# Kernel tuning notes

Measured on AMD Instinct MI355X. Metric: run time of the kernel, lower is better.

The kernel has to match this reference:

```python
import jax, jax.numpy as jnp
import numpy as np
from jax import lax

START = 0  # label_dict['<START>']
END = 8    # label_dict['<END>']
NEG = -10000.0


def setup_inputs() -> dict:
    key = jax.random.key(0)
    k1, k2, k3 = jax.random.split(key, 3)
    B, S, C = 8192, 512, 9
    emission = jax.random.normal(k1, (B, S, C), dtype=jnp.float32)
    # transition_matrix ~ normal, then START row / END column masked to -10000
    T = jax.random.normal(k2, (C, C), dtype=jnp.float32)
    T = T.at[START, :].set(NEG).at[:, END].set(NEG)
    labels = jax.random.randint(k3, (B, S), 0, 8, dtype=jnp.int32)
    mask = jnp.ones((B, S), dtype=jnp.int32)
    return {"emission": emission, "transition": T, "labels": labels, "mask": mask}


def _log_partition(emission, T, mask_f):
    # emission: [B,S,C], T: [C,C], mask_f: [B,S] float
    B, S, C = emission.shape
    init = jnp.full((B, C), NEG, dtype=emission.dtype).at[:, 0].set(0.0)

    def step(log_alpha, inp):
        em_t, m_t = inp  # [B,C], [B,1]
        # add[b,i,j] = log_alpha[b,i] + em_t[b,j] + T[i,j]
        add = log_alpha[:, :, None] + em_t[:, None, :] + T[None, :, :]
        new = jax.nn.logsumexp(add, axis=1)  # [B,C]
        log_alpha = new * m_t + log_alpha * (1.0 - m_t)
        return log_alpha, None

    em_sw = jnp.swapaxes(emission, 0, 1)          # [S,B,C]
    m_sw = jnp.swapaxes(mask_f, 0, 1)[:, :, None]  # [S,B,1]
    final, _ = lax.scan(step, init, (em_sw, m_sw))
    final = final + T[:, END][None, :]
    return jax.nn.logsumexp(final, axis=1)  # [B]


def _sentence_score(emission, T, labels, mask_f):
    B, S, C = emission.shape
    # prepend <START>=0 label
    labels_ext = jnp.concatenate(
        [jnp.full((B, 1), START, dtype=labels.dtype), labels], axis=1)  # [B,S+1]
    # emission score at the gold label of each position
    emit = jnp.take_along_axis(emission, labels[:, :, None].astype(jnp.int32), axis=2)[..., 0]  # [B,S]
    trans = T[labels_ext[:, :-1], labels_ext[:, 1:]]  # [B,S]
    scores = jnp.sum((emit + trans) * mask_f, axis=1)  # [B]
    lengths = jnp.sum(mask_f, axis=1).astype(jnp.int32)  # [B]
    last_label = labels_ext[jnp.arange(B), lengths]       # label at position len in ext seq
    scores = scores + T[last_label, END]
    return scores


def reference(emission, transition, labels, mask):
    mask_f = mask.astype(emission.dtype)
    log_Z = _log_partition(emission, transition, mask_f)
    gold = _sentence_score(emission, transition, labels, mask_f)
    loss = jnp.mean(log_Z - gold)
    return loss
```

## Files before the change

### kernel.cpp

```cpp
#include <hip/hip_runtime.h>


#define CC 9
#define SS 512
#define GPW 7
#define BLOCKT 64
#define NEGV (-10000.0f)

__device__ __forceinline__ float bperm_f(int idx, float v) {
    return __int_as_float(__builtin_amdgcn_ds_bpermute(idx, __float_as_int(v)));
}

struct Chunk {
    float em[8];
    int4 lab0, lab1, msk0, msk1;
};

struct CrfState {
    float q, offset, goldem, goldtr;
    int prev, len;
};

__device__ __forceinline__ void load_chunk(Chunk& c, const float* emp,
                                           const int* labp, const int* mskp, int t0) {
#pragma unroll
    for (int k = 0; k < 8; ++k) c.em[k] = emp[(t0 + k) * CC];
    c.lab0 = *(const int4*)(labp + t0);
    c.lab1 = *(const int4*)(labp + t0 + 4);
    c.msk0 = *(const int4*)(mskp + t0);
    c.msk1 = *(const int4*)(mskp + t0 + 4);
}

template <bool RENORM>
__device__ __forceinline__ void crf_step(CrfState& st, float em_t, int lab_t, int msk_t,
                                         const float* Tl, const float* ecol,
                                         int idxbase, int j) {
    float g[CC];
#pragma unroll
    for (int i = 0; i < CC; ++i) g[i] = bperm_f(idxbase + 4 * i, st.q);

    float e = __expf(em_t);
    float tv = Tl[st.prev * CC + lab_t];
    bool m = (msk_t != 0);
    st.goldtr += m ? tv : 0.0f;
    st.goldem += (m && (lab_t == j)) ? em_t : 0.0f;
    st.len += m ? 1 : 0;
    st.prev = lab_t;

    float s0 = g[0] * ecol[0];
    float s1 = g[1] * ecol[1];
    float s2 = g[2] * ecol[2];
    s0 = fmaf(g[3], ecol[3], s0);
    s1 = fmaf(g[4], ecol[4], s1);
    s2 = fmaf(g[5], ecol[5], s2);
    s0 = fmaf(g[6], ecol[6], s0);
    s1 = fmaf(g[7], ecol[7], s1);
    s2 = fmaf(g[8], ecol[8], s2);
    float s = s0 + s1 + s2;

    float nq = m ? s * e : st.q;
    if (RENORM) {
        float mx = fmaxf(fmaxf(fmaxf(g[0], g[1]), fmaxf(g[2], g[3])),
                         fmaxf(fmaxf(g[4], g[5]),
                               fmaxf(g[6], fmaxf(g[7], g[8]))));
        nq = nq / mx;
        st.offset += __logf(mx);
    }
    st.q = nq;
}

__device__ __forceinline__ void consume8(CrfState& st, const Chunk& c, const float* Tl,
                                         const float* ecol, int idxbase, int j) {
    crf_step<true >(st, c.em[0], c.lab0.x, c.msk0.x, Tl, ecol, idxbase, j);
    crf_step<false>(st, c.em[1], c.lab0.y, c.msk0.y, Tl, ecol, idxbase, j);
    crf_step<false>(st, c.em[2], c.lab0.z, c.msk0.z, Tl, ecol, idxbase, j);
    crf_step<false>(st, c.em[3], c.lab0.w, c.msk0.w, Tl, ecol, idxbase, j);
    crf_step<true >(st, c.em[4], c.lab1.x, c.msk1.x, Tl, ecol, idxbase, j);
    crf_step<false>(st, c.em[5], c.lab1.y, c.msk1.y, Tl, ecol, idxbase, j);
    crf_step<false>(st, c.em[6], c.lab1.z, c.msk1.z, Tl, ecol, idxbase, j);
    crf_step<false>(st, c.em[7], c.lab1.w, c.msk1.w, Tl, ecol, idxbase, j);
}

__global__ void zero_out_kernel(float* out) { out[0] = 0.0f; }

__global__ __launch_bounds__(BLOCKT) void crf_main(
    const float* __restrict__ emission, const float* __restrict__ transition,
    const int* __restrict__ labels, const int* __restrict__ mask,
    float* __restrict__ out, int B, float invB) {
    __shared__ float Tl[CC * CC];
    int tid = threadIdx.x;
    for (int i = tid; i < CC * CC; i += BLOCKT) Tl[i] = transition[i];
    __syncthreads();

    int lane = tid & 63;
    int grp = lane / CC;
    int j = lane - grp * CC;
    long batch = (long)blockIdx.x * GPW + grp;
    bool valid = (grp < GPW) && (batch < (long)B);
    int idxbase = (grp * CC) * 4;

    float ecol[CC];
#pragma unroll
    for (int i = 0; i < CC; ++i) ecol[i] = __expf(Tl[i * CC + j]);
    float mT8 = Tl[0 * CC + 8];
#pragma unroll
    for (int i = 1; i < CC; ++i) mT8 = fmaxf(mT8, Tl[i * CC + 8]);
    float wend = __expf(Tl[j * CC + 8] - mT8);

    float vj, vref;
    {
        float mxj = Tl[j], mx0 = Tl[0];
#pragma unroll
        for (int i = 1; i < CC; ++i) {
            mxj = fmaxf(mxj, NEGV + Tl[i * CC + j]);
            mx0 = fmaxf(mx0, NEGV + Tl[i * CC + 0]);
        }
        float sj = __expf(Tl[j] - mxj), s0 = __expf(Tl[0] - mx0);
#pragma unroll
        for (int i = 1; i < CC; ++i) {
            sj += __expf(NEGV + Tl[i * CC + j] - mxj);
            s0 += __expf(NEGV + Tl[i * CC + 0] - mx0);
        }
        vj = mxj + __logf(sj);
        vref = mx0 + __logf(s0);
    }

    size_t bidx = valid ? (size_t)batch : 0;
    const float* emp = emission + bidx * (SS * CC) + j;
    const int* labp = labels + bidx * SS;
    const int* mskp = mask + bidx * SS;

    CrfState st;
    st.q = 0.f; st.offset = 0.f; st.goldem = 0.f; st.goldtr = 0.f;
    st.prev = 0; st.len = 0;

    Chunk A, Bc;
    load_chunk(A, emp, labp, mskp, 0);
    load_chunk(Bc, emp, labp, mskp, 8);

    {
        float em0 = A.em[0];
        int lab0 = A.lab0.x;
        bool m0 = (A.msk0.x != 0);
        st.offset = m0 ? vref : 0.f;
        st.q = m0 ? __expf(vj + em0 - vref) : ((j == 0) ? 1.f : 0.f);
        st.goldtr = m0 ? Tl[lab0] : 0.f;
        st.goldem = (m0 && lab0 == j) ? em0 : 0.f;
        st.len = m0 ? 1 : 0;
        st.prev = lab0;
    }
    crf_step<false>(st, A.em[1], A.lab0.y, A.msk0.y, Tl, ecol, idxbase, j);
    crf_step<false>(st, A.em[2], A.lab0.z, A.msk0.z, Tl, ecol, idxbase, j);
    crf_step<false>(st, A.em[3], A.lab0.w, A.msk0.w, Tl, ecol, idxbase, j);
    crf_step<true >(st, A.em[4], A.lab1.x, A.msk1.x, Tl, ecol, idxbase, j);
    crf_step<false>(st, A.em[5], A.lab1.y, A.msk1.y, Tl, ecol, idxbase, j);
    crf_step<false>(st, A.em[6], A.lab1.z, A.msk1.z, Tl, ecol, idxbase, j);
    crf_step<false>(st, A.em[7], A.lab1.w, A.msk1.w, Tl, ecol, idxbase, j);

    load_chunk(A, emp, labp, mskp, 16);

    for (int c = 1; c <= 61; c += 2) {
        consume8(st, Bc, Tl, ecol, idxbase, j);
        load_chunk(Bc, emp, labp, mskp, (c + 2) * 8);
        consume8(st, A, Tl, ecol, idxbase, j);
        if (c + 3 <= 63) load_chunk(A, emp, labp, mskp, (c + 3) * 8);
    }
    consume8(st, Bc, Tl, ecol, idxbase, j);

    int lastlab = 0;
    if (st.len > 0) lastlab = labp[st.len - 1];
    float gend = Tl[lastlab * CC + 8];
    float fin = st.q * wend;
    float gpart = st.goldem + ((j == 0) ? (st.goldtr + gend) : 0.f);
    float sw = 0.f, sg = 0.f;
#pragma unroll
    for (int i = 0; i < CC; ++i) {
        sw += bperm_f(idxbase + 4 * i, fin);
        sg += bperm_f(idxbase + 4 * i, gpart);
    }
    if (valid && j == 0) {
        float logZ = st.offset + mT8 + __logf(sw);
        atomicAdd(out, (logZ - sg) * invB);
    }
}

extern "C" void kernel_launch(void* const* d_in, const int* in_sizes, int n_in,
                              void* d_out, int out_size, void* d_ws, size_t ws_size,
                              hipStream_t stream) {
    const float* emission = (const float*)d_in[0];
    const float* transition = (const float*)d_in[1];
    const int* labels = (const int*)d_in[2];
    const int* mask = (const int*)d_in[3];
    float* out = (float*)d_out;

    int B = in_sizes[2] / SS;
    float invB = 1.0f / (float)B;

    zero_out_kernel<<<1, 1, 0, stream>>>(out);
    int nblocks = (B + GPW - 1) / GPW;
    crf_main<<<nblocks, BLOCKT, 0, stream>>>(emission, transition, labels, mask,
                                             out, B, invB);
}
```

Measured before the change: 279.9 us.

## Fold CRF states onto 8 lanes, use DPP rotates, reduce per block

```diff
diff --git a/kernel.cpp b/kernel.cpp
--- a/kernel.cpp
+++ b/kernel.cpp
@@ -3,185 +3,216 @@
 
 #define CC 9
 #define SS 512
-#define GPW 7
-#define BLOCKT 64
 #define NEGV (-10000.0f)
-
-__device__ __forceinline__ float bperm_f(int idx, float v) {
-    return __int_as_float(__builtin_amdgcn_ds_bpermute(idx, __float_as_int(v)));
+#define BLOCKT 256
+#define BPW 8
+#define BPB 32
+
+template <int M>
+__device__ __forceinline__ float rotf(float v) {
+    return __int_as_float(__builtin_amdgcn_update_dpp(
+        0, __float_as_int(v), 0x120 + 2 * M, 0xF, 0xF, false));
+}
+template <int M>
+__device__ __forceinline__ int roti(int v) {
+    return __builtin_amdgcn_update_dpp(0, v, 0x120 + 2 * M, 0xF, 0xF, false);
 }
 
 struct Chunk {
     float em[8];
-    int4 lab0, lab1, msk0, msk1;
+    int lab[8];
+    int msk[8];
 };
 
-struct CrfState {
-    float q, offset, goldem, goldtr;
-    int prev, len;
+struct St {
+    float q, offset, goldtr, goldem;
+    int len, prev;
 };
 
 __device__ __forceinline__ void load_chunk(Chunk& c, const float* emp,
                                            const int* labp, const int* mskp, int t0) {
 #pragma unroll
     for (int k = 0; k < 8; ++k) c.em[k] = emp[(t0 + k) * CC];
-    c.lab0 = *(const int4*)(labp + t0);
-    c.lab1 = *(const int4*)(labp + t0 + 4);
-    c.msk0 = *(const int4*)(mskp + t0);
-    c.msk1 = *(const int4*)(mskp + t0 + 4);
+    int4 l0 = *(const int4*)(labp + t0);
+    int4 l1 = *(const int4*)(labp + t0 + 4);
+    int4 m0 = *(const int4*)(mskp + t0);
+    int4 m1 = *(const int4*)(mskp + t0 + 4);
+    c.lab[0] = l0.x; c.lab[1] = l0.y; c.lab[2] = l0.z; c.lab[3] = l0.w;
+    c.lab[4] = l1.x; c.lab[5] = l1.y; c.lab[6] = l1.z; c.lab[7] = l1.w;
+    c.msk[0] = m0.x; c.msk[1] = m0.y; c.msk[2] = m0.z; c.msk[3] = m0.w;
+    c.msk[4] = m1.x; c.msk[5] = m1.y; c.msk[6] = m1.z; c.msk[7] = m1.w;
 }
 
 template <bool RENORM>
-__device__ __forceinline__ void crf_step(CrfState& st, float em_t, int lab_t, int msk_t,
-                                         const float* Tl, const float* ecol,
-                                         int idxbase, int j) {
-    float g[CC];
-#pragma unroll
-    for (int i = 0; i < CC; ++i) g[i] = bperm_f(idxbase + 4 * i, st.q);
-
-    float e = __expf(em_t);
-    float tv = Tl[st.prev * CC + lab_t];
-    bool m = (msk_t != 0);
+__device__ __forceinline__ void crf_step(St& st, float e, float em, int lab, int msk,
+                                         float tv, const float* w, int o) {
+    float q = st.q;
+    float g1 = rotf<1>(q), g2 = rotf<2>(q), g3 = rotf<3>(q);
+    float g4 = rotf<4>(q), g5 = rotf<5>(q), g6 = rotf<6>(q), g7 = rotf<7>(q);
+    float s0 = q * w[0];
+    float s1 = g1 * w[1];
+    float s2 = g2 * w[2];
+    s0 = fmaf(g3, w[3], s0);
+    s1 = fmaf(g4, w[4], s1);
+    s2 = fmaf(g5, w[5], s2);
+    s0 = fmaf(g6, w[6], s0);
+    s1 = fmaf(g7, w[7], s1);
+    float ssum = s0 + (s1 + s2);
+    bool m = (msk != 0);
     st.goldtr += m ? tv : 0.0f;
-    st.goldem += (m && (lab_t == j)) ? em_t : 0.0f;
+    st.goldem += (m && lab == o) ? em : 0.0f;
     st.len += m ? 1 : 0;
-    st.prev = lab_t;
-
-    float s0 = g[0] * ecol[0];
-    float s1 = g[1] * ecol[1];
-    float s2 = g[2] * ecol[2];
-    s0 = fmaf(g[3], ecol[3], s0);
-    s1 = fmaf(g[4], ecol[4], s1);
-    s2 = fmaf(g[5], ecol[5], s2);
-    s0 = fmaf(g[6], ecol[6], s0);
-    s1 = fmaf(g[7], ecol[7], s1);
-    s2 = fmaf(g[8], ecol[8], s2);
-    float s = s0 + s1 + s2;
-
-    float nq = m ? s * e : st.q;
+    float nq = m ? ssum * e : q;
     if (RENORM) {
-        float mx = fmaxf(fmaxf(fmaxf(g[0], g[1]), fmaxf(g[2], g[3])),
-                         fmaxf(fmaxf(g[4], g[5]),
-                               fmaxf(g[6], fmaxf(g[7], g[8]))));
-        nq = nq / mx;
+        float mx = fmaxf(nq, rotf<1>(nq));
+        mx = fmaxf(mx, rotf<2>(mx));
+        mx = fmaxf(mx, rotf<4>(mx));
+        nq *= __builtin_amdgcn_rcpf(mx);
         st.offset += __logf(mx);
     }
     st.q = nq;
 }
 
-__device__ __forceinline__ void consume8(CrfState& st, const Chunk& c, const float* Tl,
-                                         const float* ecol, int idxbase, int j) {
-    crf_step<true >(st, c.em[0], c.lab0.x, c.msk0.x, Tl, ecol, idxbase, j);
-    crf_step<false>(st, c.em[1], c.lab0.y, c.msk0.y, Tl, ecol, idxbase, j);
-    crf_step<false>(st, c.em[2], c.lab0.z, c.msk0.z, Tl, ecol, idxbase, j);
-    crf_step<false>(st, c.em[3], c.lab0.w, c.msk0.w, Tl, ecol, idxbase, j);
-    crf_step<true >(st, c.em[4], c.lab1.x, c.msk1.x, Tl, ecol, idxbase, j);
-    crf_step<false>(st, c.em[5], c.lab1.y, c.msk1.y, Tl, ecol, idxbase, j);
-    crf_step<false>(st, c.em[6], c.lab1.z, c.msk1.z, Tl, ecol, idxbase, j);
-    crf_step<false>(st, c.em[7], c.lab1.w, c.msk1.w, Tl, ecol, idxbase, j);
-}
-
-__global__ void zero_out_kernel(float* out) { out[0] = 0.0f; }
-
-__global__ __launch_bounds__(BLOCKT) void crf_main(
+__device__ __forceinline__ void consume8(St& st, const Chunk& c, const float* Tl,
+                                         const float* w, int o) {
+    float tv[8];
+    tv[0] = Tl[st.prev * CC + c.lab[0]];
+#pragma unroll
+    for (int k = 1; k < 8; ++k) tv[k] = Tl[c.lab[k - 1] * CC + c.lab[k]];
+    st.prev = c.lab[7];
+    float e[8];
+#pragma unroll
+    for (int k = 0; k < 8; ++k) e[k] = __expf(c.em[k]);
+    crf_step<true >(st, e[0], c.em[0], c.lab[0], c.msk[0], tv[0], w, o);
+    crf_step<false>(st, e[1], c.em[1], c.lab[1], c.msk[1], tv[1], w, o);
+    crf_step<false>(st, e[2], c.em[2], c.lab[2], c.msk[2], tv[2], w, o);
+    crf_step<false>(st, e[3], c.em[3], c.lab[3], c.msk[3], tv[3], w, o);
+    crf_step<true >(st, e[4], c.em[4], c.lab[4], c.msk[4], tv[4], w, o);
+    crf_step<false>(st, e[5], c.em[5], c.lab[5], c.msk[5], tv[5], w, o);
+    crf_step<false>(st, e[6], c.em[6], c.lab[6], c.msk[6], tv[6], w, o);
+    crf_step<false>(st, e[7], c.em[7], c.lab[7], c.msk[7], tv[7], w, o);
+}
+
+__global__ __launch_bounds__(BLOCKT, 1) void crf_main(
     const float* __restrict__ emission, const float* __restrict__ transition,
     const int* __restrict__ labels, const int* __restrict__ mask,
     float* __restrict__ out, int B, float invB) {
     __shared__ float Tl[CC * CC];
+    __shared__ float blocksum;
     int tid = threadIdx.x;
+    if (tid == 0) blocksum = 0.0f;
     for (int i = tid; i < CC * CC; i += BLOCKT) Tl[i] = transition[i];
     __syncthreads();
 
-    int lane = tid & 63;
-    int grp = lane / CC;
-    int j = lane - grp * CC;
-    long batch = (long)blockIdx.x * GPW + grp;
-    bool valid = (grp < GPW) && (batch < (long)B);
-    int idxbase = (grp * CC) * 4;
-
-    float ecol[CC];
-#pragma unroll
-    for (int i = 0; i < CC; ++i) ecol[i] = __expf(Tl[i * CC + j]);
-    float mT8 = Tl[0 * CC + 8];
+    int lane = tid & 63, wv = tid >> 6;
+    int pos = lane & 15, row = lane >> 4;
+    int par = pos & 1, s = pos >> 1;
+    int o = s;
+    long batch = (long)blockIdx.x * BPB + wv * BPW + row * 2 + par;
+    bool valid = batch < (long)B;
+    size_t bidx = valid ? (size_t)batch : 0;
+
+    int ssrc[8];
+    ssrc[0] = s;
+    ssrc[1] = roti<1>(s); ssrc[2] = roti<2>(s); ssrc[3] = roti<3>(s);
+    ssrc[4] = roti<4>(s); ssrc[5] = roti<5>(s); ssrc[6] = roti<6>(s);
+    ssrc[7] = roti<7>(s);
+    float wmain[8], wf[8];
+#pragma unroll
+    for (int m = 0; m < 8; ++m) {
+        int is_ = ssrc[m];
+        wmain[m] = __expf(Tl[is_ * CC + o]);
+        wf[m] = __expf(Tl[(is_ == 0 ? 8 : is_) * CC + o]);
+    }
+
+    float mT8 = Tl[8];
 #pragma unroll
     for (int i = 1; i < CC; ++i) mT8 = fmaxf(mT8, Tl[i * CC + 8]);
-    float wend = __expf(Tl[j * CC + 8] - mT8);
-
-    float vj, vref;
+    float wend = __expf(Tl[o * CC + 8] - mT8);
+
+    int colq = (s == 0) ? 8 : s;
+    float v, vref;
     {
-        float mxj = Tl[j], mx0 = Tl[0];
+        float mx1 = Tl[colq], mx2 = Tl[1];
 #pragma unroll
         for (int i = 1; i < CC; ++i) {
-            mxj = fmaxf(mxj, NEGV + Tl[i * CC + j]);
-            mx0 = fmaxf(mx0, NEGV + Tl[i * CC + 0]);
+            mx1 = fmaxf(mx1, NEGV + Tl[i * CC + colq]);
+            mx2 = fmaxf(mx2, NEGV + Tl[i * CC + 1]);
         }
-        float sj = __expf(Tl[j] - mxj), s0 = __expf(Tl[0] - mx0);
+        float a1 = __expf(Tl[colq] - mx1), a2 = __expf(Tl[1] - mx2);
 #pragma unroll
         for (int i = 1; i < CC; ++i) {
-            sj += __expf(NEGV + Tl[i * CC + j] - mxj);
-            s0 += __expf(NEGV + Tl[i * CC + 0] - mx0);
+            a1 += __expf(NEGV + Tl[i * CC + colq] - mx1);
+            a2 += __expf(NEGV + Tl[i * CC + 1] - mx2);
         }
-        vj = mxj + __logf(sj);
-        vref = mx0 + __logf(s0);
-    }
-
-    size_t bidx = valid ? (size_t)batch : 0;
-    const float* emp = emission + bidx * (SS * CC) + j;
+        v = mx1 + __logf(a1);
+        vref = mx2 + __logf(a2);
+    }
+
+    const float* emp = emission + bidx * (SS * CC) + o;
     const int* labp = labels + bidx * SS;
     const int* mskp = mask + bidx * SS;
-
-    CrfState st;
-    st.q = 0.f; st.offset = 0.f; st.goldem = 0.f; st.goldtr = 0.f;
-    st.prev = 0; st.len = 0;
+    float em8 = emission[bidx * (SS * CC) + 8];
 
     Chunk A, Bc;
     load_chunk(A, emp, labp, mskp, 0);
     load_chunk(Bc, emp, labp, mskp, 8);
 
+    St st;
+    st.q = 0.f; st.offset = 0.f; st.goldtr = 0.f; st.goldem = 0.f;
+    st.len = 0; st.prev = 0;
+
     {
-        float em0 = A.em[0];
-        int lab0 = A.lab0.x;
-        bool m0 = (A.msk0.x != 0);
-        st.offset = m0 ? vref : 0.f;
-        st.q = m0 ? __expf(vj + em0 - vref) : ((j == 0) ? 1.f : 0.f);
-        st.goldtr = m0 ? Tl[lab0] : 0.f;
-        st.goldem = (m0 && lab0 == j) ? em0 : 0.f;
+        bool m0 = (A.msk[0] != 0);
+        float em0q = (s == 0) ? em8 : A.em[0];
+        st.q = m0 ? __expf(v + em0q - vref) : 0.0f;
+        st.offset = m0 ? vref : 0.0f;
+        st.goldtr = m0 ? Tl[A.lab[0]] : 0.0f;
+        st.goldem = (m0 && A.lab[0] == o) ? A.em[0] : 0.0f;
         st.len = m0 ? 1 : 0;
-        st.prev = lab0;
-    }
-    crf_step<false>(st, A.em[1], A.lab0.y, A.msk0.y, Tl, ecol, idxbase, j);
-    crf_step<false>(st, A.em[2], A.lab0.z, A.msk0.z, Tl, ecol, idxbase, j);
-    crf_step<false>(st, A.em[3], A.lab0.w, A.msk0.w, Tl, ecol, idxbase, j);
-    crf_step<true >(st, A.em[4], A.lab1.x, A.msk1.x, Tl, ecol, idxbase, j);
-    crf_step<false>(st, A.em[5], A.lab1.y, A.msk1.y, Tl, ecol, idxbase, j);
-    crf_step<false>(st, A.em[6], A.lab1.z, A.msk1.z, Tl, ecol, idxbase, j);
-    crf_step<false>(st, A.em[7], A.lab1.w, A.msk1.w, Tl, ecol, idxbase, j);
-
+    }
+    {
+        float tv[8];
+#pragma unroll
+        for (int k = 1; k < 8; ++k) tv[k] = Tl[A.lab[k - 1] * CC + A.lab[k]];
+        st.prev = A.lab[7];
+        float e[8];
+#pragma unroll
+        for (int k = 1; k < 8; ++k) e[k] = __expf(A.em[k]);
+        crf_step<false>(st, e[1], A.em[1], A.lab[1], A.msk[1], tv[1], wf, o);
+        crf_step<false>(st, e[2], A.em[2], A.lab[2], A.msk[2], tv[2], wmain, o);
+        crf_step<false>(st, e[3], A.em[3], A.lab[3], A.msk[3], tv[3], wmain, o);
+        crf_step<true >(st, e[4], A.em[4], A.lab[4], A.msk[4], tv[4], wmain, o);
+        crf_step<false>(st, e[5], A.em[5], A.lab[5], A.msk[5], tv[5], wmain, o);
+        crf_step<false>(st, e[6], A.em[6], A.lab[6], A.msk[6], tv[6], wmain, o);
+        crf_step<false>(st, e[7], A.em[7], A.lab[7], A.msk[7], tv[7], wmain, o);
+    }
     load_chunk(A, emp, labp, mskp, 16);
 
     for (int c = 1; c <= 61; c += 2) {
-        consume8(st, Bc, Tl, ecol, idxbase, j);
+        consume8(st, Bc, Tl, wmain, o);
         load_chunk(Bc, emp, labp, mskp, (c + 2) * 8);
-        consume8(st, A, Tl, ecol, idxbase, j);
+        consume8(st, A, Tl, wmain, o);
         if (c + 3 <= 63) load_chunk(A, emp, labp, mskp, (c + 3) * 8);
     }
-    consume8(st, Bc, Tl, ecol, idxbase, j);
-
-    int lastlab = 0;
-    if (st.len > 0) lastlab = labp[st.len - 1];
+    consume8(st, Bc, Tl, wmain, o);
+
+    int lastlab = (st.len > 0) ? labp[st.len - 1] : 0;
     float gend = Tl[lastlab * CC + 8];
     float fin = st.q * wend;
-    float gpart = st.goldem + ((j == 0) ? (st.goldtr + gend) : 0.f);
-    float sw = 0.f, sg = 0.f;
-#pragma unroll
-    for (int i = 0; i < CC; ++i) {
-        sw += bperm_f(idxbase + 4 * i, fin);
-        sg += bperm_f(idxbase + 4 * i, gpart);
-    }
-    if (valid && j == 0) {
+    float sw = fin + rotf<1>(fin);
+    sw = sw + rotf<2>(sw);
+    sw = sw + rotf<4>(sw);
+    float gpart = st.goldem + ((s == 0) ? (st.goldtr + gend) : 0.0f);
+    float sg = gpart + rotf<1>(gpart);
+    sg = sg + rotf<2>(sg);
+    sg = sg + rotf<4>(sg);
+    if (valid && s == 0) {
         float logZ = st.offset + mT8 + __logf(sw);
-        atomicAdd(out, (logZ - sg) * invB);
-    }
+        atomicAdd(&blocksum, (logZ - sg) * invB);
+    }
+    __syncthreads();
+    if (tid == 0) atomicAdd(out, blocksum);
 }
 
 extern "C" void kernel_launch(void* const* d_in, const int* in_sizes, int n_in,
@@ -196,8 +227,8 @@
     int B = in_sizes[2] / SS;
     float invB = 1.0f / (float)B;
 
-    zero_out_kernel<<<1, 1, 0, stream>>>(out);
-    int nblocks = (B + GPW - 1) / GPW;
+    hipMemsetAsync(out, 0, sizeof(float) * out_size, stream);
+    int nblocks = (B + BPB - 1) / BPB;
     crf_main<<<nblocks, BLOCKT, 0, stream>>>(emission, transition, labels, mask,
                                              out, B, invB);
 }
```

Measured after the change: 249.3 us. -10.9%, faster.
